# Kernel optimization log

Measured on AMD Instinct MI355X. Metric: run time of the kernel, lower is better.

Reference implementation:

```python
import jax, jax.numpy as jnp
import numpy as np

B, T, C = 4, 2048, 1024
H = 16
D = C // H  # head_dim = 64


def setup_inputs() -> dict:
    key = jax.random.key(0)
    ks = jax.random.split(key, 9)
    s = 1.0 / np.sqrt(C)
    return {
        "x": jax.random.normal(ks[0], (B, T, C), dtype=jnp.float32),
        "wq": jax.random.uniform(ks[1], (C, C), jnp.float32, -s, s),
        "bq": jax.random.uniform(ks[2], (C,), jnp.float32, -s, s),
        "wk": jax.random.uniform(ks[3], (C, C), jnp.float32, -s, s),
        "bk": jax.random.uniform(ks[4], (C,), jnp.float32, -s, s),
        "wv": jax.random.uniform(ks[5], (C, C), jnp.float32, -s, s),
        "bv": jax.random.uniform(ks[6], (C,), jnp.float32, -s, s),
        "wo": jax.random.uniform(ks[7], (C, C), jnp.float32, -s, s),
        "bo": jax.random.uniform(ks[8], (C,), jnp.float32, -s, s),
    }


def reference(x, wq, bq, wk, bk, wv, bv, wo, bo):
    # Linear layers (torch convention: y = x @ W.T + b)
    q = x @ wq.T + bq  # [B,T,C]
    k = x @ wk.T + bk
    v = x @ wv.T + bv
    # split heads -> [B,H,T,D]
    q = q.reshape(B, T, H, D).transpose(0, 2, 1, 3)
    k = k.reshape(B, T, H, D).transpose(0, 2, 1, 3)
    v = v.reshape(B, T, H, D).transpose(0, 2, 1, 3)
    scores = jnp.einsum('bhqd,bhkd->bhqk', q, k) / jnp.sqrt(jnp.float32(D))
    causal = jnp.tril(jnp.ones((T, T), dtype=bool))  # position i attends to j<=i
    scores = jnp.where(causal, scores, -jnp.inf)
    attn = jax.nn.softmax(scores, axis=-1)
    # dropout p=0.0 (eval / identity)
    out = jnp.einsum('bhqk,bhkd->bhqd', attn, v)  # [B,H,T,D]
    out = out.transpose(0, 2, 1, 3).reshape(B, T, C)
    return out @ wo.T + bo
```

## Files before the change

kernel.cpp:

```cpp
#include <hip/hip_runtime.h>
#include <stdint.h>

#define B_DIM 4
#define T_DIM 2048
#define C_DIM 1024
#define H_DIM 16
#define D_DIM 64
#define M_DIM (B_DIM * T_DIM)
#define QK_SCALE 0.18033688011112042f

typedef float f32x4 __attribute__((ext_vector_type(4)));
typedef float f32x16 __attribute__((ext_vector_type(16)));
typedef short bf16x8 __attribute__((ext_vector_type(8)));
typedef unsigned short u16;
typedef u16 u16x8 __attribute__((ext_vector_type(8)));

static __device__ __forceinline__ u16 f2b(float f) {
  uint32_t r;
  asm("v_cvt_pk_bf16_f32 %0, %1, %1" : "=v"(r) : "v"(f));
  return (u16)r;
}
static __device__ __forceinline__ uint32_t f2b2(float a, float b) {
  uint32_t r;
  asm("v_cvt_pk_bf16_f32 %0, %1, %2" : "=v"(r) : "v"(a), "v"(b));
  return r;
}

static __device__ __forceinline__ void gl_lds16(const u16* g, u16* l) {
  __builtin_amdgcn_global_load_lds(
      (const __attribute__((address_space(1))) void*)g,
      (__attribute__((address_space(3))) void*)l, 16, 0, 0);
}

__global__ void k_cvt(const float* __restrict__ src, u16* __restrict__ dst, int n4) {
  int i = blockIdx.x * blockDim.x + threadIdx.x;
  if (i < n4) {
    float4 v = ((const float4*)src)[i];
    uint2 o;
    o.x = f2b2(v.x, v.y);
    o.y = f2b2(v.z, v.w);
    ((uint2*)dst)[i] = o;
  }
}

__global__ void k_cvtw(const float* __restrict__ s0, const float* __restrict__ s1,
                       const float* __restrict__ s2, const float* __restrict__ s3,
                       u16* __restrict__ d0, u16* __restrict__ d1,
                       u16* __restrict__ d2, u16* __restrict__ d3) {
  int i = blockIdx.x * blockDim.x + threadIdx.x;
  int seg = i >> 18;
  int j = i & ((1 << 18) - 1);
  const float* s = seg == 0 ? s0 : seg == 1 ? s1 : seg == 2 ? s2 : s3;
  u16* d = seg == 0 ? d0 : seg == 1 ? d1 : seg == 2 ? d2 : d3;
  float4 v = ((const float4*)s)[j];
  uint2 o;
  o.x = f2b2(v.x, v.y);
  o.y = f2b2(v.z, v.w);
  ((uint2*)d)[j] = o;
}

__global__ __launch_bounds__(256) void k_gemm_qkv(
    const u16* __restrict__ A,
    const u16* __restrict__ w0, const u16* __restrict__ w1, const u16* __restrict__ w2,
    const float* __restrict__ b0, const float* __restrict__ b1, const float* __restrict__ b2,
    u16* __restrict__ Qo, u16* __restrict__ Ko, u16* __restrict__ Vo) {
  __shared__ u16 As[128 * 32];
  __shared__ u16 Bs[128 * 32];
  const int tid = threadIdx.x;
  const int l = tid & 63;
  const int w = tid >> 6;
  const int wr = w >> 1, wc = w & 1;
  const int seg = blockIdx.x >> 3;
  const int brow = blockIdx.y * 128, bcol = (blockIdx.x & 7) * 128;
  const int lrow = l & 15, lk = l >> 4;
  const int K = C_DIM;

  const u16* Bw = seg == 0 ? w0 : seg == 1 ? w1 : w2;
  const float* bias = seg == 0 ? b0 : seg == 1 ? b1 : b2;
  u16* Out = seg == 0 ? Qo : seg == 1 ? Ko : Vo;
  const float scale = seg == 0 ? QK_SCALE : 1.f;

  f32x4 acc[4][4];
  for (int m = 0; m < 4; ++m)
    for (int n = 0; n < 4; ++n)
      acc[m][n] = (f32x4){0.f, 0.f, 0.f, 0.f};

  for (int kt = 0; kt < K; kt += 32) {
    __syncthreads();
    {
      int slot = tid;
      int r0 = slot >> 2, c0 = slot & 3;
      gl_lds16(A + (size_t)(brow + r0) * K + kt + c0 * 8, As + slot * 8);
      gl_lds16(Bw + (size_t)(bcol + r0) * K + kt + c0 * 8, Bs + slot * 8);
      int slot2 = slot + 256;
      int r1 = slot2 >> 2, c1 = slot2 & 3;
      gl_lds16(A + (size_t)(brow + r1) * K + kt + c1 * 8, As + slot2 * 8);
      gl_lds16(Bw + (size_t)(bcol + r1) * K + kt + c1 * 8, Bs + slot2 * 8);
    }
    asm volatile("s_waitcnt vmcnt(0)" ::: "memory");
    __syncthreads();

    bf16x8 af[4], bfr[4];
#pragma unroll
    for (int m = 0; m < 4; ++m)
      af[m] = *(const bf16x8*)(As + (wr * 64 + m * 16 + lrow) * 32 + lk * 8);
#pragma unroll
    for (int n = 0; n < 4; ++n)
      bfr[n] = *(const bf16x8*)(Bs + (wc * 64 + n * 16 + lrow) * 32 + lk * 8);
#pragma unroll
    for (int m = 0; m < 4; ++m) {
#pragma unroll
      for (int n = 0; n < 4; ++n)
        acc[m][n] = __builtin_amdgcn_mfma_f32_16x16x32_bf16(af[m], bfr[n], acc[m][n], 0, 0, 0);
    }
  }

#pragma unroll
  for (int m = 0; m < 4; ++m) {
    int rg0 = brow + wr * 64 + m * 16 + lk * 4;
#pragma unroll
    for (int n = 0; n < 4; ++n) {
      int cg = bcol + wc * 64 + n * 16 + lrow;
      float bv = bias[cg];
#pragma unroll
      for (int i = 0; i < 4; ++i) {
        int rg = rg0 + i;
        float val = (acc[m][n][i] + bv) * scale;
        int bb = rg >> 11, tt = rg & (T_DIM - 1);
        int hh = cg >> 6, dd = cg & 63;
        Out[(((size_t)bb * H_DIM + hh) * T_DIM + tt) * D_DIM + dd] = f2b(val);
      }
    }
  }
}

__global__ __launch_bounds__(256) void k_gemm_proj(
    const u16* __restrict__ A, const u16* __restrict__ Bw,
    const float* __restrict__ bias, float* __restrict__ Cout) {
  __shared__ u16 As[128 * 32];
  __shared__ u16 Bs[128 * 32];
  const int tid = threadIdx.x;
  const int l = tid & 63;
  const int w = tid >> 6;
  const int wr = w >> 1, wc = w & 1;
  const int brow = blockIdx.y * 128, bcol = blockIdx.x * 128;
  const int lrow = l & 15, lk = l >> 4;
  const int K = C_DIM, N = C_DIM;

  f32x4 acc[4][4];
  for (int m = 0; m < 4; ++m)
    for (int n = 0; n < 4; ++n)
      acc[m][n] = (f32x4){0.f, 0.f, 0.f, 0.f};

  for (int kt = 0; kt < K; kt += 32) {
    __syncthreads();
    {
      int slot = tid;
      int r0 = slot >> 2, c0 = slot & 3;
      gl_lds16(A + (size_t)(brow + r0) * K + kt + c0 * 8, As + slot * 8);
      gl_lds16(Bw + (size_t)(bcol + r0) * K + kt + c0 * 8, Bs + slot * 8);
      int slot2 = slot + 256;
      int r1 = slot2 >> 2, c1 = slot2 & 3;
      gl_lds16(A + (size_t)(brow + r1) * K + kt + c1 * 8, As + slot2 * 8);
      gl_lds16(Bw + (size_t)(bcol + r1) * K + kt + c1 * 8, Bs + slot2 * 8);
    }
    asm volatile("s_waitcnt vmcnt(0)" ::: "memory");
    __syncthreads();

    bf16x8 af[4], bfr[4];
#pragma unroll
    for (int m = 0; m < 4; ++m)
      af[m] = *(const bf16x8*)(As + (wr * 64 + m * 16 + lrow) * 32 + lk * 8);
#pragma unroll
    for (int n = 0; n < 4; ++n)
      bfr[n] = *(const bf16x8*)(Bs + (wc * 64 + n * 16 + lrow) * 32 + lk * 8);
#pragma unroll
    for (int m = 0; m < 4; ++m) {
#pragma unroll
      for (int n = 0; n < 4; ++n)
        acc[m][n] = __builtin_amdgcn_mfma_f32_16x16x32_bf16(af[m], bfr[n], acc[m][n], 0, 0, 0);
    }
  }

#pragma unroll
  for (int m = 0; m < 4; ++m) {
    int rg0 = brow + wr * 64 + m * 16 + lk * 4;
#pragma unroll
    for (int n = 0; n < 4; ++n) {
      int cg = bcol + wc * 64 + n * 16 + lrow;
      float bv = bias[cg];
#pragma unroll
      for (int i = 0; i < 4; ++i)
        Cout[(size_t)(rg0 + i) * N + cg] = acc[m][n][i] + bv;
    }
  }
}

__global__ __launch_bounds__(256) void k_transpose(
    const u16* __restrict__ V, u16* __restrict__ Vt) {
  __shared__ u16 tile[64][65];
  const int tid = threadIdx.x;
  const int bh = blockIdx.y;
  const int t0 = blockIdx.x * 64;
  const size_t ibase = (size_t)bh * T_DIM * D_DIM + (size_t)t0 * D_DIM;
  const size_t obase = (size_t)bh * D_DIM * T_DIM + t0;

#pragma unroll
  for (int it = 0; it < 2; ++it) {
    int row = (tid >> 3) + it * 32;
    int blk = tid & 7;
    u16x8 v = *(const u16x8*)(V + ibase + (size_t)row * D_DIM + blk * 8);
#pragma unroll
    for (int j = 0; j < 8; ++j) tile[row][blk * 8 + j] = v[j];
  }
  __syncthreads();
#pragma unroll
  for (int it = 0; it < 2; ++it) {
    int d = (tid >> 3) + it * 32;
    int blk = tid & 7;
    u16x8 v;
#pragma unroll
    for (int j = 0; j < 8; ++j) v[j] = tile[blk * 8 + j][d];
    *(u16x8*)(Vt + obase + (size_t)d * T_DIM + blk * 8) = v;
  }
}

__global__ __launch_bounds__(512) void k_attn(
    const u16* __restrict__ Q, const u16* __restrict__ Kg,
    const u16* __restrict__ Vt, u16* __restrict__ O) {
  __shared__ u16 Ks[2][64 * 64];
  __shared__ u16 Vs[2][64 * 64];

  const int tid = threadIdx.x;
  const int l = tid & 63;
  const int w = tid >> 6;
  const int bh = blockIdx.x;
  const int qb = 7 - blockIdx.y;
  const int q0 = qb * 256;
  const int ql = l & 31;
  const int hi = l >> 5;
  const int r0 = q0 + w * 32;
  const int qg = r0 + ql;

  const size_t qkbase = (size_t)bh * T_DIM * D_DIM;
  const size_t vtbase = (size_t)bh * D_DIM * T_DIM;

  const int sr = tid >> 3, sc = tid & 7;
  const int kcol = (sc ^ (sr & 7)) * 8;

#define STAGE(buf, kt)                                                                  \
  {                                                                                     \
    gl_lds16(Kg + qkbase + (size_t)((kt) * 64 + sr) * D_DIM + kcol, Ks[buf] + tid * 8); \
    gl_lds16(Vt + vtbase + (size_t)sr * T_DIM + (kt) * 64 + kcol, Vs[buf] + tid * 8);   \
  }

  bf16x8 qf[4];
#pragma unroll
  for (int kk = 0; kk < 4; ++kk)
    qf[kk] = *(const bf16x8*)(Q + qkbase + (size_t)qg * D_DIM + kk * 16 + hi * 8);

  f32x16 oacc[2];
#pragma unroll
  for (int dt = 0; dt < 2; ++dt)
#pragma unroll
    for (int r = 0; r < 16; ++r) oacc[dt][r] = 0.f;
  float m_run = -1e30f, l_run = 0.f;

  const int tdiag = r0 >> 6;
  const int nkt = (q0 >> 6) + 4;

  STAGE(0, 0);

  for (int kt = 0; kt < nkt; ++kt) {
    const int cur = kt & 1;
    if (kt + 1 < nkt) {
      STAGE(cur ^ 1, kt + 1);
      asm volatile("s_waitcnt vmcnt(2)" ::: "memory");
    } else {
      asm volatile("s_waitcnt vmcnt(0)" ::: "memory");
    }
    __syncthreads();

    if (kt <= tdiag) {
      f32x16 s[2];
#pragma unroll
      for (int a = 0; a < 2; ++a)
#pragma unroll
        for (int r = 0; r < 16; ++r) s[a][r] = 0.f;

#pragma unroll
      for (int kk = 0; kk < 4; ++kk) {
#pragma unroll
        for (int a = 0; a < 2; ++a) {
          int row = a * 32 + ql;
          int blk = (kk * 2 + hi) ^ (row & 7);
          bf16x8 kf = *(const bf16x8*)(Ks[cur] + row * 64 + blk * 8);
          s[a] = __builtin_amdgcn_mfma_f32_32x32x16_bf16(kf, qf[kk], s[a], 0, 0, 0);
        }
      }

      if (kt == tdiag) {
#pragma unroll
        for (int a = 0; a < 2; ++a) {
#pragma unroll
          for (int r = 0; r < 16; ++r) {
            int kv = kt * 64 + a * 32 + (r & 3) + 8 * (r >> 2) + 4 * hi;
            if (kv > qg) s[a][r] = -1e30f;
          }
        }
      }

      float t[16];
#pragma unroll
      for (int r = 0; r < 16; ++r) t[r] = fmaxf(s[0][r], s[1][r]);
#pragma unroll
      for (int r = 0; r < 8; ++r) t[r] = fmaxf(t[r], t[r + 8]);
#pragma unroll
      for (int r = 0; r < 4; ++r) t[r] = fmaxf(t[r], t[r + 4]);
      float pm = fmaxf(fmaxf(t[0], t[1]), fmaxf(t[2], t[3]));
      pm = fmaxf(pm, __shfl_xor(pm, 32, 64));

      if (__any(pm > m_run + 8.f)) {
        float mn = fmaxf(m_run, pm);
        float sc_ = exp2f(m_run - mn);
        m_run = mn;
        l_run *= sc_;
#pragma unroll
        for (int dt = 0; dt < 2; ++dt)
#pragma unroll
          for (int r = 0; r < 16; ++r) oacc[dt][r] *= sc_;
      }

      float rs0 = 0.f, rs1 = 0.f, rs2 = 0.f, rs3 = 0.f;
#pragma unroll
      for (int a = 0; a < 2; ++a) {
#pragma unroll
        for (int r = 0; r < 16; ++r) {
          float p = exp2f(s[a][r] - m_run);
          s[a][r] = p;
          if ((r & 3) == 0) rs0 += p;
          else if ((r & 3) == 1) rs1 += p;
          else if ((r & 3) == 2) rs2 += p;
          else rs3 += p;
        }
      }
      float rs = (rs0 + rs1) + (rs2 + rs3);
      rs += __shfl_xor(rs, 32, 64);
      l_run += rs;

#pragma unroll
      for (int kk = 0; kk < 4; ++kk) {
        const int a = kk >> 1;
        const int base = (kk & 1) * 8;
        union { uint32_t wd[4]; bf16x8 v; } pf;
#pragma unroll
        for (int i = 0; i < 2; ++i) {
          uint32_t Aw = f2b2(s[a][base + 2 * i], s[a][base + 2 * i + 1]);
          uint32_t Bw = f2b2(s[a][base + 4 + 2 * i], s[a][base + 5 + 2 * i]);
          uint32_t As_ = (uint32_t)__shfl_xor((int)Aw, 32, 64);
          uint32_t Bs_ = (uint32_t)__shfl_xor((int)Bw, 32, 64);
          pf.wd[i] = hi ? Bs_ : Aw;
          pf.wd[2 + i] = hi ? Bw : As_;
        }
#pragma unroll
        for (int dt = 0; dt < 2; ++dt) {
          int row = dt * 32 + ql;
          int blk = (kk * 2 + hi) ^ (row & 7);
          bf16x8 vf = *(const bf16x8*)(Vs[cur] + row * 64 + blk * 8);
          oacc[dt] = __builtin_amdgcn_mfma_f32_32x32x16_bf16(vf, pf.v, oacc[dt], 0, 0, 0);
        }
      }
    }
    __syncthreads();
  }

  const int bb = bh >> 4, hh = bh & 15;
  const float inv = 1.f / l_run;
  u16* orow = O + ((size_t)bb * T_DIM + qg) * C_DIM + hh * D_DIM;
#pragma unroll
  for (int dt = 0; dt < 2; ++dt) {
#pragma unroll
    for (int g = 0; g < 4; ++g) {
      uint2 val;
      val.x = f2b2(oacc[dt][g * 4 + 0] * inv, oacc[dt][g * 4 + 1] * inv);
      val.y = f2b2(oacc[dt][g * 4 + 2] * inv, oacc[dt][g * 4 + 3] * inv);
      *(uint2*)(orow + dt * 32 + g * 8 + 4 * hi) = val;
    }
  }
}

extern "C" void kernel_launch(void* const* d_in, const int* in_sizes, int n_in,
                              void* d_out, int out_size, void* d_ws, size_t ws_size,
                              hipStream_t stream) {
  (void)in_sizes; (void)n_in; (void)out_size; (void)ws_size;
  const float* x  = (const float*)d_in[0];
  const float* wq = (const float*)d_in[1];
  const float* bq = (const float*)d_in[2];
  const float* wk = (const float*)d_in[3];
  const float* bk = (const float*)d_in[4];
  const float* wv = (const float*)d_in[5];
  const float* bv = (const float*)d_in[6];
  const float* wo = (const float*)d_in[7];
  const float* bo = (const float*)d_in[8];
  float* out = (float*)d_out;

  u16* xb  = (u16*)d_ws;
  u16* wqb = xb + (size_t)M_DIM * C_DIM;
  u16* wkb = wqb + (size_t)C_DIM * C_DIM;
  u16* wvb = wkb + (size_t)C_DIM * C_DIM;
  u16* wob = wvb + (size_t)C_DIM * C_DIM;
  u16* Qb  = wob + (size_t)C_DIM * C_DIM;
  u16* Kb  = Qb + (size_t)M_DIM * C_DIM;
  u16* Vb  = Kb + (size_t)M_DIM * C_DIM;
  u16* Vtb = Vb + (size_t)M_DIM * C_DIM;
  u16* Ob  = Vb;

  int n4x = M_DIM * C_DIM / 4;
  k_cvt<<<(n4x + 255) / 256, 256, 0, stream>>>(x, xb, n4x);
  k_cvtw<<<4096, 256, 0, stream>>>(wq, wk, wv, wo, wqb, wkb, wvb, wob);

  k_gemm_qkv<<<dim3(24, M_DIM / 128), 256, 0, stream>>>(
      xb, wqb, wkb, wvb, bq, bk, bv, Qb, Kb, Vb);

  k_transpose<<<dim3(T_DIM / 64, B_DIM * H_DIM), 256, 0, stream>>>(Vb, Vtb);
  k_attn<<<dim3(B_DIM * H_DIM, 8), 512, 0, stream>>>(Qb, Kb, Vtb, Ob);
  k_gemm_proj<<<dim3(C_DIM / 128, M_DIM / 128), 256, 0, stream>>>(Ob, wob, bo, out);
}
```

Measured before the change: 199.1 us.

## Write V transposed from QKV GEMM, merge conversions, use 128-wide KV tiles

The QKV GEMM epilogue now writes V directly in transposed [B,H,D,T] layout with packed stores, which removes the separate transpose kernel and its extra global round trip. The x and weight conversion kernels are merged into one launch. The attention kernel stages 128 keys per iteration, processing two 64-key halves per barrier, which halves the number of sync and wait points at the cost of doubled LDS use. The extra LDS may lower occupancy.

```diff
diff --git a/kernel.cpp b/kernel.cpp
--- a/kernel.cpp
+++ b/kernel.cpp
@@ -25,6 +25,12 @@
   asm("v_cvt_pk_bf16_f32 %0, %1, %2" : "=v"(r) : "v"(a), "v"(b));
   return r;
 }
+static __device__ __forceinline__ float xhalf_max(float x) {
+  return fmaxf(x, __shfl_xor(x, 32, 64));
+}
+static __device__ __forceinline__ float xhalf_sum(float x) {
+  return x + __shfl_xor(x, 32, 64);
+}
 
 static __device__ __forceinline__ void gl_lds16(const u16* g, u16* l) {
   __builtin_amdgcn_global_load_lds(
@@ -32,26 +38,25 @@
       (__attribute__((address_space(3))) void*)l, 16, 0, 0);
 }
 
-__global__ void k_cvt(const float* __restrict__ src, u16* __restrict__ dst, int n4) {
+__global__ void k_cvt_all(const float* __restrict__ x,
+                          const float* __restrict__ s0, const float* __restrict__ s1,
+                          const float* __restrict__ s2, const float* __restrict__ s3,
+                          u16* __restrict__ dx,
+                          u16* __restrict__ d0, u16* __restrict__ d1,
+                          u16* __restrict__ d2, u16* __restrict__ d3) {
   int i = blockIdx.x * blockDim.x + threadIdx.x;
-  if (i < n4) {
-    float4 v = ((const float4*)src)[i];
-    uint2 o;
-    o.x = f2b2(v.x, v.y);
-    o.y = f2b2(v.z, v.w);
-    ((uint2*)dst)[i] = o;
-  }
-}
-
-__global__ void k_cvtw(const float* __restrict__ s0, const float* __restrict__ s1,
-                       const float* __restrict__ s2, const float* __restrict__ s3,
-                       u16* __restrict__ d0, u16* __restrict__ d1,
-                       u16* __restrict__ d2, u16* __restrict__ d3) {
-  int i = blockIdx.x * blockDim.x + threadIdx.x;
-  int seg = i >> 18;
-  int j = i & ((1 << 18) - 1);
-  const float* s = seg == 0 ? s0 : seg == 1 ? s1 : seg == 2 ? s2 : s3;
-  u16* d = seg == 0 ? d0 : seg == 1 ? d1 : seg == 2 ? d2 : d3;
+  const float* s;
+  u16* d;
+  int j;
+  if (i < (1 << 21)) {
+    s = x; d = dx; j = i;
+  } else {
+    int k = i - (1 << 21);
+    int seg = k >> 18;
+    j = k & ((1 << 18) - 1);
+    s = seg == 0 ? s0 : seg == 1 ? s1 : seg == 2 ? s2 : s3;
+    d = seg == 0 ? d0 : seg == 1 ? d1 : seg == 2 ? d2 : d3;
+  }
   float4 v = ((const float4*)s)[j];
   uint2 o;
   o.x = f2b2(v.x, v.y);
@@ -63,7 +68,7 @@
     const u16* __restrict__ A,
     const u16* __restrict__ w0, const u16* __restrict__ w1, const u16* __restrict__ w2,
     const float* __restrict__ b0, const float* __restrict__ b1, const float* __restrict__ b2,
-    u16* __restrict__ Qo, u16* __restrict__ Ko, u16* __restrict__ Vo) {
+    u16* __restrict__ Qo, u16* __restrict__ Ko, u16* __restrict__ Vto) {
   __shared__ u16 As[128 * 32];
   __shared__ u16 Bs[128 * 32];
   const int tid = threadIdx.x;
@@ -77,7 +82,6 @@
 
   const u16* Bw = seg == 0 ? w0 : seg == 1 ? w1 : w2;
   const float* bias = seg == 0 ? b0 : seg == 1 ? b1 : b2;
-  u16* Out = seg == 0 ? Qo : seg == 1 ? Ko : Vo;
   const float scale = seg == 0 ? QK_SCALE : 1.f;
 
   f32x4 acc[4][4];
@@ -118,17 +122,26 @@
 #pragma unroll
   for (int m = 0; m < 4; ++m) {
     int rg0 = brow + wr * 64 + m * 16 + lk * 4;
+    int bb = rg0 >> 11, tt0 = rg0 & (T_DIM - 1);
 #pragma unroll
     for (int n = 0; n < 4; ++n) {
       int cg = bcol + wc * 64 + n * 16 + lrow;
       float bv = bias[cg];
-#pragma unroll
-      for (int i = 0; i < 4; ++i) {
-        int rg = rg0 + i;
-        float val = (acc[m][n][i] + bv) * scale;
-        int bb = rg >> 11, tt = rg & (T_DIM - 1);
-        int hh = cg >> 6, dd = cg & 63;
-        Out[(((size_t)bb * H_DIM + hh) * T_DIM + tt) * D_DIM + dd] = f2b(val);
+      int hh = cg >> 6, dd = cg & 63;
+      if (seg == 2) {
+        float v0 = acc[m][n][0] + bv, v1 = acc[m][n][1] + bv;
+        float v2 = acc[m][n][2] + bv, v3 = acc[m][n][3] + bv;
+        uint2 pv;
+        pv.x = f2b2(v0, v1);
+        pv.y = f2b2(v2, v3);
+        *(uint2*)(Vto + (((size_t)bb * H_DIM + hh) * D_DIM + dd) * T_DIM + tt0) = pv;
+      } else {
+        u16* Out = seg == 0 ? Qo : Ko;
+#pragma unroll
+        for (int i = 0; i < 4; ++i) {
+          float val = (acc[m][n][i] + bv) * scale;
+          Out[(((size_t)bb * H_DIM + hh) * T_DIM + tt0 + i) * D_DIM + dd] = f2b(val);
+        }
       }
     }
   }
@@ -196,40 +209,11 @@
   }
 }
 
-__global__ __launch_bounds__(256) void k_transpose(
-    const u16* __restrict__ V, u16* __restrict__ Vt) {
-  __shared__ u16 tile[64][65];
-  const int tid = threadIdx.x;
-  const int bh = blockIdx.y;
-  const int t0 = blockIdx.x * 64;
-  const size_t ibase = (size_t)bh * T_DIM * D_DIM + (size_t)t0 * D_DIM;
-  const size_t obase = (size_t)bh * D_DIM * T_DIM + t0;
-
-#pragma unroll
-  for (int it = 0; it < 2; ++it) {
-    int row = (tid >> 3) + it * 32;
-    int blk = tid & 7;
-    u16x8 v = *(const u16x8*)(V + ibase + (size_t)row * D_DIM + blk * 8);
-#pragma unroll
-    for (int j = 0; j < 8; ++j) tile[row][blk * 8 + j] = v[j];
-  }
-  __syncthreads();
-#pragma unroll
-  for (int it = 0; it < 2; ++it) {
-    int d = (tid >> 3) + it * 32;
-    int blk = tid & 7;
-    u16x8 v;
-#pragma unroll
-    for (int j = 0; j < 8; ++j) v[j] = tile[blk * 8 + j][d];
-    *(u16x8*)(Vt + obase + (size_t)d * T_DIM + blk * 8) = v;
-  }
-}
-
 __global__ __launch_bounds__(512) void k_attn(
     const u16* __restrict__ Q, const u16* __restrict__ Kg,
     const u16* __restrict__ Vt, u16* __restrict__ O) {
-  __shared__ u16 Ks[2][64 * 64];
-  __shared__ u16 Vs[2][64 * 64];
+  __shared__ u16 Ks[2][128 * 64];
+  __shared__ u16 Vs[2][64 * 128];
 
   const int tid = threadIdx.x;
   const int l = tid & 63;
@@ -247,11 +231,17 @@
 
   const int sr = tid >> 3, sc = tid & 7;
   const int kcol = (sc ^ (sr & 7)) * 8;
-
-#define STAGE(buf, kt)                                                                  \
-  {                                                                                     \
-    gl_lds16(Kg + qkbase + (size_t)((kt) * 64 + sr) * D_DIM + kcol, Ks[buf] + tid * 8); \
-    gl_lds16(Vt + vtbase + (size_t)sr * T_DIM + (kt) * 64 + kcol, Vs[buf] + tid * 8);   \
+  const int vr = tid >> 4, vc = tid & 15;
+  const int vcol = (vc ^ (vr & 7)) * 8;
+
+#define STAGE(buf, kt)                                                                    \
+  {                                                                                       \
+    gl_lds16(Kg + qkbase + (size_t)((kt) * 128 + sr) * D_DIM + kcol, Ks[buf] + tid * 8);  \
+    gl_lds16(Kg + qkbase + (size_t)((kt) * 128 + 64 + sr) * D_DIM + kcol,                 \
+             Ks[buf] + 4096 + tid * 8);                                                   \
+    gl_lds16(Vt + vtbase + (size_t)vr * T_DIM + (kt) * 128 + vcol, Vs[buf] + tid * 8);    \
+    gl_lds16(Vt + vtbase + (size_t)(vr + 32) * T_DIM + (kt) * 128 + vcol,                 \
+             Vs[buf] + 4096 + tid * 8);                                                   \
   }
 
   bf16x8 qf[4];
@@ -266,8 +256,8 @@
     for (int r = 0; r < 16; ++r) oacc[dt][r] = 0.f;
   float m_run = -1e30f, l_run = 0.f;
 
-  const int tdiag = r0 >> 6;
-  const int nkt = (q0 >> 6) + 4;
+  const int tdiag64 = r0 >> 6;
+  const int nkt = (q0 >> 7) + 2;
 
   STAGE(0, 0);
 
@@ -275,99 +265,103 @@
     const int cur = kt & 1;
     if (kt + 1 < nkt) {
       STAGE(cur ^ 1, kt + 1);
-      asm volatile("s_waitcnt vmcnt(2)" ::: "memory");
+      asm volatile("s_waitcnt vmcnt(4)" ::: "memory");
     } else {
       asm volatile("s_waitcnt vmcnt(0)" ::: "memory");
     }
     __syncthreads();
 
-    if (kt <= tdiag) {
-      f32x16 s[2];
-#pragma unroll
-      for (int a = 0; a < 2; ++a)
-#pragma unroll
-        for (int r = 0; r < 16; ++r) s[a][r] = 0.f;
-
-#pragma unroll
-      for (int kk = 0; kk < 4; ++kk) {
+#pragma unroll
+    for (int h2 = 0; h2 < 2; ++h2) {
+      const int kt64 = kt * 2 + h2;
+      if (kt64 <= tdiag64) {
+        const u16* Kt = Ks[cur] + h2 * 4096;
+        f32x16 s[2];
+#pragma unroll
+        for (int a = 0; a < 2; ++a)
+#pragma unroll
+          for (int r = 0; r < 16; ++r) s[a][r] = 0.f;
+
+#pragma unroll
+        for (int kk = 0; kk < 4; ++kk) {
+#pragma unroll
+          for (int a = 0; a < 2; ++a) {
+            int row = a * 32 + ql;
+            int blk = (kk * 2 + hi) ^ (row & 7);
+            bf16x8 kf = *(const bf16x8*)(Kt + row * 64 + blk * 8);
+            s[a] = __builtin_amdgcn_mfma_f32_32x32x16_bf16(kf, qf[kk], s[a], 0, 0, 0);
+          }
+        }
+
+        if (kt64 == tdiag64) {
+#pragma unroll
+          for (int a = 0; a < 2; ++a) {
+#pragma unroll
+            for (int r = 0; r < 16; ++r) {
+              int kv = kt64 * 64 + a * 32 + (r & 3) + 8 * (r >> 2) + 4 * hi;
+              if (kv > qg) s[a][r] = -1e30f;
+            }
+          }
+        }
+
+        float t[16];
+#pragma unroll
+        for (int r = 0; r < 16; ++r) t[r] = fmaxf(s[0][r], s[1][r]);
+#pragma unroll
+        for (int r = 0; r < 8; ++r) t[r] = fmaxf(t[r], t[r + 8]);
+#pragma unroll
+        for (int r = 0; r < 4; ++r) t[r] = fmaxf(t[r], t[r + 4]);
+        float pm = fmaxf(fmaxf(t[0], t[1]), fmaxf(t[2], t[3]));
+        pm = xhalf_max(pm);
+
+        if (__any(pm > m_run + 8.f)) {
+          float mn = fmaxf(m_run, pm);
+          float sc_ = exp2f(m_run - mn);
+          m_run = mn;
+          l_run *= sc_;
+#pragma unroll
+          for (int dt = 0; dt < 2; ++dt)
+#pragma unroll
+            for (int r = 0; r < 16; ++r) oacc[dt][r] *= sc_;
+        }
+
+        float rs0 = 0.f, rs1 = 0.f, rs2 = 0.f, rs3 = 0.f;
 #pragma unroll
         for (int a = 0; a < 2; ++a) {
-          int row = a * 32 + ql;
-          int blk = (kk * 2 + hi) ^ (row & 7);
-          bf16x8 kf = *(const bf16x8*)(Ks[cur] + row * 64 + blk * 8);
-          s[a] = __builtin_amdgcn_mfma_f32_32x32x16_bf16(kf, qf[kk], s[a], 0, 0, 0);
-        }
-      }
-
-      if (kt == tdiag) {
-#pragma unroll
-        for (int a = 0; a < 2; ++a) {
 #pragma unroll
           for (int r = 0; r < 16; ++r) {
-            int kv = kt * 64 + a * 32 + (r & 3) + 8 * (r >> 2) + 4 * hi;
-            if (kv > qg) s[a][r] = -1e30f;
+            float p = exp2f(s[a][r] - m_run);
+            s[a][r] = p;
+            if ((r & 3) == 0) rs0 += p;
+            else if ((r & 3) == 1) rs1 += p;
+            else if ((r & 3) == 2) rs2 += p;
+            else rs3 += p;
           }
         }
-      }
-
-      float t[16];
-#pragma unroll
-      for (int r = 0; r < 16; ++r) t[r] = fmaxf(s[0][r], s[1][r]);
-#pragma unroll
-      for (int r = 0; r < 8; ++r) t[r] = fmaxf(t[r], t[r + 8]);
-#pragma unroll
-      for (int r = 0; r < 4; ++r) t[r] = fmaxf(t[r], t[r + 4]);
-      float pm = fmaxf(fmaxf(t[0], t[1]), fmaxf(t[2], t[3]));
-      pm = fmaxf(pm, __shfl_xor(pm, 32, 64));
-
-      if (__any(pm > m_run + 8.f)) {
-        float mn = fmaxf(m_run, pm);
-        float sc_ = exp2f(m_run - mn);
-        m_run = mn;
-        l_run *= sc_;
-#pragma unroll
-        for (int dt = 0; dt < 2; ++dt)
-#pragma unroll
-          for (int r = 0; r < 16; ++r) oacc[dt][r] *= sc_;
-      }
-
-      float rs0 = 0.f, rs1 = 0.f, rs2 = 0.f, rs3 = 0.f;
-#pragma unroll
-      for (int a = 0; a < 2; ++a) {
-#pragma unroll
-        for (int r = 0; r < 16; ++r) {
-          float p = exp2f(s[a][r] - m_run);
-          s[a][r] = p;
-          if ((r & 3) == 0) rs0 += p;
-          else if ((r & 3) == 1) rs1 += p;
-          else if ((r & 3) == 2) rs2 += p;
-          else rs3 += p;
-        }
-      }
-      float rs = (rs0 + rs1) + (rs2 + rs3);
-      rs += __shfl_xor(rs, 32, 64);
-      l_run += rs;
-
-#pragma unroll
-      for (int kk = 0; kk < 4; ++kk) {
-        const int a = kk >> 1;
-        const int base = (kk & 1) * 8;
-        union { uint32_t wd[4]; bf16x8 v; } pf;
-#pragma unroll
-        for (int i = 0; i < 2; ++i) {
-          uint32_t Aw = f2b2(s[a][base + 2 * i], s[a][base + 2 * i + 1]);
-          uint32_t Bw = f2b2(s[a][base + 4 + 2 * i], s[a][base + 5 + 2 * i]);
-          uint32_t As_ = (uint32_t)__shfl_xor((int)Aw, 32, 64);
-          uint32_t Bs_ = (uint32_t)__shfl_xor((int)Bw, 32, 64);
-          pf.wd[i] = hi ? Bs_ : Aw;
-          pf.wd[2 + i] = hi ? Bw : As_;
-        }
-#pragma unroll
-        for (int dt = 0; dt < 2; ++dt) {
-          int row = dt * 32 + ql;
-          int blk = (kk * 2 + hi) ^ (row & 7);
-          bf16x8 vf = *(const bf16x8*)(Vs[cur] + row * 64 + blk * 8);
-          oacc[dt] = __builtin_amdgcn_mfma_f32_32x32x16_bf16(vf, pf.v, oacc[dt], 0, 0, 0);
+        float rs = (rs0 + rs1) + (rs2 + rs3);
+        l_run += xhalf_sum(rs);
+
+#pragma unroll
+        for (int kk = 0; kk < 4; ++kk) {
+          const int a = kk >> 1;
+          const int base = (kk & 1) * 8;
+          union { uint32_t wd[4]; bf16x8 v; } pf;
+#pragma unroll
+          for (int i = 0; i < 2; ++i) {
+            uint32_t Aw = f2b2(s[a][base + 2 * i], s[a][base + 2 * i + 1]);
+            uint32_t Bw = f2b2(s[a][base + 4 + 2 * i], s[a][base + 5 + 2 * i]);
+            uint32_t As_ = (uint32_t)__shfl_xor((int)Aw, 32, 64);
+            uint32_t Bs_ = (uint32_t)__shfl_xor((int)Bw, 32, 64);
+            pf.wd[i] = hi ? Bs_ : Aw;
+            pf.wd[2 + i] = hi ? Bw : As_;
+          }
+#pragma unroll
+          for (int dt = 0; dt < 2; ++dt) {
+            int row = dt * 32 + ql;
+            int chunk = (h2 * 8) + ((kk * 2 + hi) ^ (row & 7));
+            bf16x8 vf = *(const bf16x8*)(Vs[cur] + row * 128 + chunk * 8);
+            oacc[dt] = __builtin_amdgcn_mfma_f32_32x32x16_bf16(vf, pf.v, oacc[dt], 0, 0, 0);
+          }
         }
       }
     }
@@ -411,18 +405,14 @@
   u16* wob = wvb + (size_t)C_DIM * C_DIM;
   u16* Qb  = wob + (size_t)C_DIM * C_DIM;
   u16* Kb  = Qb + (size_t)M_DIM * C_DIM;
-  u16* Vb  = Kb + (size_t)M_DIM * C_DIM;
-  u16* Vtb = Vb + (size_t)M_DIM * C_DIM;
-  u16* Ob  = Vb;
-
-  int n4x = M_DIM * C_DIM / 4;
-  k_cvt<<<(n4x + 255) / 256, 256, 0, stream>>>(x, xb, n4x);
-  k_cvtw<<<4096, 256, 0, stream>>>(wq, wk, wv, wo, wqb, wkb, wvb, wob);
+  u16* Vtb = Kb + (size_t)M_DIM * C_DIM;
+  u16* Ob  = Vtb + (size_t)M_DIM * C_DIM;
+
+  k_cvt_all<<<12288, 256, 0, stream>>>(x, wq, wk, wv, wo, xb, wqb, wkb, wvb, wob);
 
   k_gemm_qkv<<<dim3(24, M_DIM / 128), 256, 0, stream>>>(
-      xb, wqb, wkb, wvb, bq, bk, bv, Qb, Kb, Vb);
-
-  k_transpose<<<dim3(T_DIM / 64, B_DIM * H_DIM), 256, 0, stream>>>(Vb, Vtb);
+      xb, wqb, wkb, wvb, bq, bk, bv, Qb, Kb, Vtb);
+
   k_attn<<<dim3(B_DIM * H_DIM, 8), 512, 0, stream>>>(Qb, Kb, Vtb, Ob);
   k_gemm_proj<<<dim3(C_DIM / 128, M_DIM / 128), 256, 0, stream>>>(Ob, wob, bo, out);
 }
```

Result: no change. 198.4 us (-0.4%).
